# Kernel optimization log

Hardware: AMD Instinct MI355X
Metric: run time of the kernel (lower is better)

## Reference

```python
import jax, jax.numpy as jnp
import numpy as np

STEP_SIZE = 0.01  # init kwarg step_size

def _quad_grad(A, b, x):
    # grad of per-node quadratic: 2*A_n @ x_n + b_n ; shapes [N,D,D],[N,D],[N,D]
    return 2.0 * jnp.einsum('nij,nj->ni', A, x) + b

def setup_inputs() -> dict:
    key = jax.random.key(0)
    kA, kb, kx, ke = jax.random.split(key, 4)
    N, D, E = 20000, 64, 320000
    A = jax.random.normal(kA, (N, D, D), dtype=jnp.float32)
    b = jax.random.normal(kb, (N, D), dtype=jnp.float32)
    x = jax.random.normal(kx, (N, D), dtype=jnp.float32)
    edge_index = jax.random.randint(ke, (2, E), 0, N, dtype=jnp.int64)
    return {"A": A, "b": b, "x": x, "edge_index": edge_index, "num_layers": 10}

def reference(A, b, x, edge_index, num_layers):
    N, D = x.shape
    src, dst = edge_index[0], edge_index[1]
    # push-sum column-stochastic mixing weights: 1/out_degree incl. self-loop
    deg = jnp.ones((N,), x.dtype).at[src].add(1.0)
    inv_deg = (1.0 / deg)[:, None]  # [N,1]

    def mix(z):  # z: [N,F]
        msg = z[src] * inv_deg[src]  # gather + weight
        agg = jax.ops.segment_sum(msg, dst, num_segments=N)
        return agg + z * inv_deg  # self-loop term

    y = _quad_grad(A, b, x)
    u = x
    v = jnp.ones((N, 1), x.dtype)
    x0 = x
    x1 = x0
    for _ in range(num_layers):
        u = mix(u - STEP_SIZE * y)          # conv on u
        v = mix(v)                           # conv on v (push-sum weight)
        x1 = u * (1.0 / v)                   # inv_v * u
        g1 = _quad_grad(A, b, x1)
        g0 = _quad_grad(A, b, x0)
        y = mix(y) + g1 - g0                 # conv on y + gradient tracking
        x0 = x1
    comm_cost = jnp.asarray(3 * num_layers * src.shape[0], dtype=jnp.int64)
    return x1, comm_cost
```

## Files before the change

### kernel.cpp

```cpp
#include <hip/hip_runtime.h>
#include <hip/hip_bf16.h>
#include <hip/hip_fp16.h>

#define STEP 0.01f
#define D 64
#define NUM_LAYERS 10

union H4 { uint2 u; __half h[4]; };
union H8 { uint4 u; __half2 h2[4]; __half h[8]; };
union HI { __half2 h; int i; };

typedef float f32x2 __attribute__((ext_vector_type(2)));


__global__ void k_setup(float* __restrict__ degf, int* __restrict__ degd, int N) {
    int n = blockIdx.x * blockDim.x + threadIdx.x;
    if (n < N) { degf[n] = 1.0f; degd[n] = 0; }
}

__global__ void k_deg2(const int* __restrict__ ei, float* __restrict__ degf,
                       int* __restrict__ degd, int E) {
    int e = blockIdx.x * blockDim.x + threadIdx.x;
    if (e < E) {
        unsafeAtomicAdd(&degf[ei[e]], 1.0f);
        atomicAdd(&degd[ei[E + e]], 1);
    }
}

__global__ __launch_bounds__(1024) void k_scan(
        const int* __restrict__ degd, const float* __restrict__ degf,
        int* __restrict__ row_ptr, int* __restrict__ cursor,
        float* __restrict__ invdeg, int N, int E) {
    __shared__ int part[1024];
    int tid = threadIdx.x;
    int chunk = (N + 1023) / 1024;
    int lo = tid * chunk, hi = min(lo + chunk, N);
    int s = 0;
    for (int i = lo; i < hi; ++i) s += degd[i];
    part[tid] = s;
    __syncthreads();
    for (int off = 1; off < 1024; off <<= 1) {
        int v = (tid >= off) ? part[tid - off] : 0;
        __syncthreads();
        part[tid] += v;
        __syncthreads();
    }
    int base = (tid == 0) ? 0 : part[tid - 1];
    for (int i = lo; i < hi; ++i) {
        row_ptr[i] = base;
        cursor[i] = base;
        base += degd[i];
        invdeg[i] = 1.0f / degf[i];
    }
    if (tid == 1023) row_ptr[N] = E;
}

__global__ void k_scatter(const int* __restrict__ ei, int* __restrict__ cursor,
                          int* __restrict__ col, int E) {
    int e = blockIdx.x * blockDim.x + threadIdx.x;
    if (e < E) {
        int pos = atomicAdd(&cursor[ei[E + e]], 1);
        col[pos] = ei[e];
    }
}


__global__ __launch_bounds__(256) void k_init(
        const float* __restrict__ A, const float* __restrict__ b,
        const float* __restrict__ x, const float* __restrict__ invdeg,
        unsigned char* __restrict__ Ah8, __half2* __restrict__ msg,
        float* __restrict__ vw, float* __restrict__ x0, int N) {
    __shared__ __align__(16) float sx[D];
    __shared__ float syv[D];
    int n = blockIdx.x, t = threadIdx.x;
    int lane = t & 63, w = t >> 6, colgrp = lane & 15;
    if (t < D) sx[t] = x[(size_t)n * D + t];
    __syncthreads();
    const float* An = A + (size_t)n * D * D;
    unsigned char* A8n = Ah8 + (size_t)n * D * D;
    float4 xr = ((const float4*)sx)[colgrp];
    int rbase = w * 16 + (lane >> 4);
#pragma unroll
    for (int g = 0; g < 4; ++g) {
        int row = rbase + g * 4;
        float4 a = ((const float4*)(An + (size_t)row * D))[colgrp];
        int d8 = __builtin_amdgcn_cvt_pk_fp8_f32(a.x, a.y, 0, false);
        d8 = __builtin_amdgcn_cvt_pk_fp8_f32(a.z, a.w, d8, true);
        ((unsigned int*)(A8n + (size_t)row * D))[colgrp] = (unsigned int)d8;
        float p = a.x * xr.x + a.y * xr.y + a.z * xr.z + a.w * xr.w;
        p += __shfl_xor(p, 1);
        p += __shfl_xor(p, 2);
        p += __shfl_xor(p, 4);
        p += __shfl_xor(p, 8);
        if (colgrp == 0) syv[row] = 2.0f * p + b[(size_t)n * D + row];
    }
    __syncthreads();
    if (t < D) {
        float wd = invdeg[n];
        float xv = sx[t];
        float yv = syv[t];
        msg[(size_t)n * D + t] = __floats2half2_rn((xv - STEP * yv) * wd, yv * wd);
        x0[(size_t)n * D + t] = xv;
        if (t == 0) vw[n] = wd;
    }
}


__global__ __launch_bounds__(256) void k_layer(
        const unsigned char* __restrict__ Ah8,
        const int* __restrict__ row_ptr, const int* __restrict__ col,
        const __half2* __restrict__ msg, const float* __restrict__ vw,
        const float* __restrict__ invdeg,
        __half2* __restrict__ msgn, float* __restrict__ vwn,
        float* __restrict__ x0, float* __restrict__ xout,
        int last_idx, float comm, int N) {
    __shared__ float su[4][D];
    __shared__ float sy[4][D];
    __shared__ float sv[4];
    __shared__ __align__(16) float sdx[D];
    __shared__ float sun[D];
    __shared__ float sytot[D];
    __shared__ float syn[D];
    __shared__ float svn;

    int n = blockIdx.x, t = threadIdx.x;
    int lane = t & 63, w = t >> 6;
    int j = lane >> 4, q4 = lane & 15;

    int rs = row_ptr[n], re = row_ptr[n + 1];
    __half2 hz = __floats2half2_rn(0.f, 0.f);
    __half2 ac0 = hz, ac1 = hz, ac2 = hz, ac3 = hz;
    float av = 0.0f;
    for (int base = rs + w * 8; base < re; base += 32) {
        int e0 = base + (j << 1), e1 = e0 + 1;
        bool b0 = e0 < re, b1 = e1 < re;
        int s0 = 0, s1 = 0;
        if (b0) s0 = col[e0];
        if (b1) s1 = col[e1];
        H8 m0, m1;
        m0.u = make_uint4(0u, 0u, 0u, 0u);
        m1.u = make_uint4(0u, 0u, 0u, 0u);
        float w0 = 0.f, w1 = 0.f;
        if (b0) m0.u = ((const uint4*)(msg + (size_t)s0 * D))[q4];
        if (b1) m1.u = ((const uint4*)(msg + (size_t)s1 * D))[q4];
        if (b0 && q4 == 0) w0 = vw[s0];
        if (b1 && q4 == 0) w1 = vw[s1];
        ac0 = __hadd2(ac0, m0.h2[0]);
        ac1 = __hadd2(ac1, m0.h2[1]);
        ac2 = __hadd2(ac2, m0.h2[2]);
        ac3 = __hadd2(ac3, m0.h2[3]);
        ac0 = __hadd2(ac0, m1.h2[0]);
        ac1 = __hadd2(ac1, m1.h2[1]);
        ac2 = __hadd2(ac2, m1.h2[2]);
        ac3 = __hadd2(ac3, m1.h2[3]);
        av += w0 + w1;
    }
    {
        HI a, s;
        a.h = ac0; s.i = __shfl_xor(a.i, 16); a.h = __hadd2(a.h, s.h);
        s.i = __shfl_xor(a.i, 32); ac0 = __hadd2(a.h, s.h);
        a.h = ac1; s.i = __shfl_xor(a.i, 16); a.h = __hadd2(a.h, s.h);
        s.i = __shfl_xor(a.i, 32); ac1 = __hadd2(a.h, s.h);
        a.h = ac2; s.i = __shfl_xor(a.i, 16); a.h = __hadd2(a.h, s.h);
        s.i = __shfl_xor(a.i, 32); ac2 = __hadd2(a.h, s.h);
        a.h = ac3; s.i = __shfl_xor(a.i, 16); a.h = __hadd2(a.h, s.h);
        s.i = __shfl_xor(a.i, 32); ac3 = __hadd2(a.h, s.h);
    }
    av += __shfl_xor(av, 16);
    av += __shfl_xor(av, 32);
    if (j == 0) {
        float2 f0 = __half22float2(ac0);
        float2 f1 = __half22float2(ac1);
        float2 f2 = __half22float2(ac2);
        float2 f3 = __half22float2(ac3);
        ((float4*)su[w])[q4] = make_float4(f0.x, f1.x, f2.x, f3.x);
        ((float4*)sy[w])[q4] = make_float4(f0.y, f1.y, f2.y, f3.y);
        if (q4 == 0) sv[w] = av;
    }
    __syncthreads();

    if (w == 0) {
        size_t off = (size_t)n * D + lane;
        float2 self = __half22float2(msg[off]);
        float ut = su[0][lane] + su[1][lane] + su[2][lane] + su[3][lane] + self.x;
        float yt = sy[0][lane] + sy[1][lane] + sy[2][lane] + sy[3][lane] + self.y;
        float vt = sv[0] + sv[1] + sv[2] + sv[3] + vw[n];
        float x1 = ut / vt;
        sdx[lane] = x1 - x0[off];
        x0[off] = x1;
        if (xout) xout[off] = x1;
        sun[lane] = ut;
        sytot[lane] = yt;
        if (lane == 0) svn = vt;
    }
    __syncthreads();

    {
        const uint2* Ahp = (const uint2*)(Ah8 + (size_t)n * D * D);
        int cb = (t & 7) * 8;
        int r0 = t >> 3;
        uint2 a0 = Ahp[t];
        uint2 a1 = Ahp[256 + t];
        float p0 = 0.0f, p1 = 0.0f;
        f32x2 q;
        q = __builtin_amdgcn_cvt_pk_f32_fp8((int)a0.x, false);
        p0 += q.x * sdx[cb + 0] + q.y * sdx[cb + 1];
        q = __builtin_amdgcn_cvt_pk_f32_fp8((int)a0.x, true);
        p0 += q.x * sdx[cb + 2] + q.y * sdx[cb + 3];
        q = __builtin_amdgcn_cvt_pk_f32_fp8((int)a0.y, false);
        p0 += q.x * sdx[cb + 4] + q.y * sdx[cb + 5];
        q = __builtin_amdgcn_cvt_pk_f32_fp8((int)a0.y, true);
        p0 += q.x * sdx[cb + 6] + q.y * sdx[cb + 7];
        q = __builtin_amdgcn_cvt_pk_f32_fp8((int)a1.x, false);
        p1 += q.x * sdx[cb + 0] + q.y * sdx[cb + 1];
        q = __builtin_amdgcn_cvt_pk_f32_fp8((int)a1.x, true);
        p1 += q.x * sdx[cb + 2] + q.y * sdx[cb + 3];
        q = __builtin_amdgcn_cvt_pk_f32_fp8((int)a1.y, false);
        p1 += q.x * sdx[cb + 4] + q.y * sdx[cb + 5];
        q = __builtin_amdgcn_cvt_pk_f32_fp8((int)a1.y, true);
        p1 += q.x * sdx[cb + 6] + q.y * sdx[cb + 7];
        p0 += __shfl_xor(p0, 1); p1 += __shfl_xor(p1, 1);
        p0 += __shfl_xor(p0, 2); p1 += __shfl_xor(p1, 2);
        p0 += __shfl_xor(p0, 4); p1 += __shfl_xor(p1, 4);
        if ((lane & 7) == 0) {
            syn[r0]      = sytot[r0]      + 2.0f * p0;
            syn[32 + r0] = sytot[32 + r0] + 2.0f * p1;
        }
    }
    __syncthreads();

    if (t < D) {
        float wd = invdeg[n];
        float ynf = syn[t];
        msgn[(size_t)n * D + t] = __floats2half2_rn((sun[t] - STEP * ynf) * wd, ynf * wd);
        if (t == 0) vwn[n] = svn * wd;
    }
    if (xout && n == 0 && t == 0) xout[last_idx] = comm;
}


extern "C" void kernel_launch(void* const* d_in, const int* in_sizes, int n_in,
                              void* d_out, int out_size, void* d_ws, size_t ws_size,
                              hipStream_t stream) {
    const float* A  = (const float*)d_in[0];
    const float* b  = (const float*)d_in[1];
    const float* x  = (const float*)d_in[2];
    const int*   ei = (const int*)d_in[3];

    const int N = in_sizes[1] / D;
    const int E = in_sizes[3] / 2;
    const size_t ND = (size_t)N * D;

    char* ws = (char*)d_ws;
    unsigned char* Ah8 = (unsigned char*)ws;
    __half2* msg0 = (__half2*)(ws + ND * D);
    __half2* msg1 = msg0 + ND;
    float* x0   = (float*)(msg1 + ND);
    float* vw0  = x0 + ND;
    float* vw1  = vw0 + N;
    float* invdeg = vw1 + N;
    float* degf = invdeg + N;
    int* degd    = (int*)(degf + N);
    int* row_ptr = degd + N;
    int* cursor  = row_ptr + N + 4;
    int* col     = cursor + N;

    k_setup<<<(N + 255) / 256, 256, 0, stream>>>(degf, degd, N);
    k_deg2<<<(E + 255) / 256, 256, 0, stream>>>(ei, degf, degd, E);
    k_scan<<<1, 1024, 0, stream>>>(degd, degf, row_ptr, cursor, invdeg, N, E);
    k_scatter<<<(E + 255) / 256, 256, 0, stream>>>(ei, cursor, col, E);
    k_init<<<N, 256, 0, stream>>>(A, b, x, invdeg, Ah8, msg0, vw0, x0, N);

    float comm = (float)(3 * NUM_LAYERS * E);
    __half2 *mc = msg0, *mn = msg1;
    float *vc = vw0, *vn = vw1;
    for (int l = 0; l < NUM_LAYERS; ++l) {
        float* xout = (l == NUM_LAYERS - 1) ? (float*)d_out : nullptr;
        k_layer<<<N, 256, 0, stream>>>(Ah8, row_ptr, col, mc, vc, invdeg,
                                       mn, vn, x0, xout, out_size - 1, comm, N);
        __half2* tm = mc; mc = mn; mn = tm;
        float* tv = vc; vc = vn; vn = tv;
    }
}
```

Before: 910.3 us.

## Precompute push-sum weight mixing for all layers in separate lightweight kernels

The scalar push-sum weight v does not depend on node features, so its ten mixing steps now run up front in a small one-thread-per-node CSR kernel that stores 1/v per layer. The main layer kernel no longer gathers vw per edge or reduces it across waves, and it multiplies by the precomputed reciprocal instead of dividing. It also hoists the self-message and x0 loads to the start of the kernel so they overlap with the edge gather. The cost is ten extra small launches with serial per-thread edge loops, plus an extra N*10 buffer in the workspace.

```diff
diff --git a/kernel.cpp b/kernel.cpp
--- a/kernel.cpp
+++ b/kernel.cpp
@@ -65,11 +65,25 @@
 }
 
 
+__global__ void k_vmix(const int* __restrict__ row_ptr, const int* __restrict__ col,
+                       const float* __restrict__ invdeg, const float* __restrict__ w,
+                       float* __restrict__ wn, float* __restrict__ rvt, int N) {
+    int n = blockIdx.x * blockDim.x + threadIdx.x;
+    if (n < N) {
+        int rs = row_ptr[n], re = row_ptr[n + 1];
+        float s = w[n];
+        for (int e = rs; e < re; ++e) s += w[col[e]];
+        rvt[n] = 1.0f / s;
+        wn[n] = s * invdeg[n];
+    }
+}
+
+
 __global__ __launch_bounds__(256) void k_init(
         const float* __restrict__ A, const float* __restrict__ b,
         const float* __restrict__ x, const float* __restrict__ invdeg,
         unsigned char* __restrict__ Ah8, __half2* __restrict__ msg,
-        float* __restrict__ vw, float* __restrict__ x0, int N) {
+        float* __restrict__ x0, int N) {
     __shared__ __align__(16) float sx[D];
     __shared__ float syv[D];
     int n = blockIdx.x, t = threadIdx.x;
@@ -101,7 +115,6 @@
         float yv = syv[t];
         msg[(size_t)n * D + t] = __floats2half2_rn((xv - STEP * yv) * wd, yv * wd);
         x0[(size_t)n * D + t] = xv;
-        if (t == 0) vw[n] = wd;
     }
 }
 
@@ -109,28 +122,35 @@
 __global__ __launch_bounds__(256) void k_layer(
         const unsigned char* __restrict__ Ah8,
         const int* __restrict__ row_ptr, const int* __restrict__ col,
-        const __half2* __restrict__ msg, const float* __restrict__ vw,
+        const __half2* __restrict__ msg, const float* __restrict__ rvt,
         const float* __restrict__ invdeg,
-        __half2* __restrict__ msgn, float* __restrict__ vwn,
+        __half2* __restrict__ msgn,
         float* __restrict__ x0, float* __restrict__ xout,
         int last_idx, float comm, int N) {
     __shared__ float su[4][D];
     __shared__ float sy[4][D];
-    __shared__ float sv[4];
     __shared__ __align__(16) float sdx[D];
     __shared__ float sun[D];
     __shared__ float sytot[D];
     __shared__ float syn[D];
-    __shared__ float svn;
 
     int n = blockIdx.x, t = threadIdx.x;
     int lane = t & 63, w = t >> 6;
     int j = lane >> 4, q4 = lane & 15;
 
+    size_t off = (size_t)n * D + lane;
+    float rv = rvt[n];
+    float invd = invdeg[n];
+    float2 self = {0.f, 0.f};
+    float x0v = 0.f;
+    if (w == 0) {
+        self = __half22float2(msg[off]);
+        x0v = x0[off];
+    }
+
     int rs = row_ptr[n], re = row_ptr[n + 1];
     __half2 hz = __floats2half2_rn(0.f, 0.f);
     __half2 ac0 = hz, ac1 = hz, ac2 = hz, ac3 = hz;
-    float av = 0.0f;
     for (int base = rs + w * 8; base < re; base += 32) {
         int e0 = base + (j << 1), e1 = e0 + 1;
         bool b0 = e0 < re, b1 = e1 < re;
@@ -140,11 +160,8 @@
         H8 m0, m1;
         m0.u = make_uint4(0u, 0u, 0u, 0u);
         m1.u = make_uint4(0u, 0u, 0u, 0u);
-        float w0 = 0.f, w1 = 0.f;
         if (b0) m0.u = ((const uint4*)(msg + (size_t)s0 * D))[q4];
         if (b1) m1.u = ((const uint4*)(msg + (size_t)s1 * D))[q4];
-        if (b0 && q4 == 0) w0 = vw[s0];
-        if (b1 && q4 == 0) w1 = vw[s1];
         ac0 = __hadd2(ac0, m0.h2[0]);
         ac1 = __hadd2(ac1, m0.h2[1]);
         ac2 = __hadd2(ac2, m0.h2[2]);
@@ -153,7 +170,6 @@
         ac1 = __hadd2(ac1, m1.h2[1]);
         ac2 = __hadd2(ac2, m1.h2[2]);
         ac3 = __hadd2(ac3, m1.h2[3]);
-        av += w0 + w1;
     }
     {
         HI a, s;
@@ -166,8 +182,6 @@
         a.h = ac3; s.i = __shfl_xor(a.i, 16); a.h = __hadd2(a.h, s.h);
         s.i = __shfl_xor(a.i, 32); ac3 = __hadd2(a.h, s.h);
     }
-    av += __shfl_xor(av, 16);
-    av += __shfl_xor(av, 32);
     if (j == 0) {
         float2 f0 = __half22float2(ac0);
         float2 f1 = __half22float2(ac1);
@@ -175,23 +189,18 @@
         float2 f3 = __half22float2(ac3);
         ((float4*)su[w])[q4] = make_float4(f0.x, f1.x, f2.x, f3.x);
         ((float4*)sy[w])[q4] = make_float4(f0.y, f1.y, f2.y, f3.y);
-        if (q4 == 0) sv[w] = av;
     }
     __syncthreads();
 
     if (w == 0) {
-        size_t off = (size_t)n * D + lane;
-        float2 self = __half22float2(msg[off]);
         float ut = su[0][lane] + su[1][lane] + su[2][lane] + su[3][lane] + self.x;
         float yt = sy[0][lane] + sy[1][lane] + sy[2][lane] + sy[3][lane] + self.y;
-        float vt = sv[0] + sv[1] + sv[2] + sv[3] + vw[n];
-        float x1 = ut / vt;
-        sdx[lane] = x1 - x0[off];
+        float x1 = ut * rv;
+        sdx[lane] = x1 - x0v;
         x0[off] = x1;
         if (xout) xout[off] = x1;
         sun[lane] = ut;
         sytot[lane] = yt;
-        if (lane == 0) svn = vt;
     }
     __syncthreads();
 
@@ -230,10 +239,8 @@
     __syncthreads();
 
     if (t < D) {
-        float wd = invdeg[n];
         float ynf = syn[t];
-        msgn[(size_t)n * D + t] = __floats2half2_rn((sun[t] - STEP * ynf) * wd, ynf * wd);
-        if (t == 0) vwn[n] = svn * wd;
+        msgn[(size_t)n * D + t] = __floats2half2_rn((sun[t] - STEP * ynf) * invd, ynf * invd);
     }
     if (xout && n == 0 && t == 0) xout[last_idx] = comm;
 }
@@ -264,21 +271,33 @@
     int* row_ptr = degd + N;
     int* cursor  = row_ptr + N + 4;
     int* col     = cursor + N;
+    float* rvtbuf = (float*)(col + E);
 
     k_setup<<<(N + 255) / 256, 256, 0, stream>>>(degf, degd, N);
     k_deg2<<<(E + 255) / 256, 256, 0, stream>>>(ei, degf, degd, E);
     k_scan<<<1, 1024, 0, stream>>>(degd, degf, row_ptr, cursor, invdeg, N, E);
     k_scatter<<<(E + 255) / 256, 256, 0, stream>>>(ei, cursor, col, E);
-    k_init<<<N, 256, 0, stream>>>(A, b, x, invdeg, Ah8, msg0, vw0, x0, N);
+
+    {
+        const float* wcur = invdeg;
+        float* wnxt = vw0;
+        for (int l = 0; l < NUM_LAYERS; ++l) {
+            k_vmix<<<(N + 255) / 256, 256, 0, stream>>>(
+                row_ptr, col, invdeg, wcur, wnxt, rvtbuf + (size_t)l * N, N);
+            const float* tw = wnxt;
+            wnxt = (wnxt == vw0) ? vw1 : vw0;
+            wcur = tw;
+        }
+    }
+
+    k_init<<<N, 256, 0, stream>>>(A, b, x, invdeg, Ah8, msg0, x0, N);
 
     float comm = (float)(3 * NUM_LAYERS * E);
     __half2 *mc = msg0, *mn = msg1;
-    float *vc = vw0, *vn = vw1;
     for (int l = 0; l < NUM_LAYERS; ++l) {
         float* xout = (l == NUM_LAYERS - 1) ? (float*)d_out : nullptr;
-        k_layer<<<N, 256, 0, stream>>>(Ah8, row_ptr, col, mc, vc, invdeg,
-                                       mn, vn, x0, xout, out_size - 1, comm, N);
+        k_layer<<<N, 256, 0, stream>>>(Ah8, row_ptr, col, mc, rvtbuf + (size_t)l * N,
+                                       invdeg, mn, x0, xout, out_size - 1, comm, N);
         __half2* tm = mc; mc = mn; mn = tm;
-        float* tv = vc; vc = vn; vn = tv;
-    }
-}
+    }
+}
```

Result: slower. 964.2 us (+5.9%).
